# Kernel optimization log

Hardware: AMD Instinct MI355X
Metric: run time of the kernel (lower is better)

Reference implementation:

```python
import jax, jax.numpy as jnp
import numpy as np

N_SUB = 4  # fixed RK4 substeps per timestep (stands in for adaptive dopri5)
HID, IN, OUT = 64, 16, 1


def setup_inputs() -> dict:
    key = jax.random.key(0)
    ks = jax.random.split(key, 8)
    B, S = 512, 1024
    return {
        "x": jax.random.normal(ks[0], (B, S, IN), dtype=jnp.float32),
        "W_in": jax.random.normal(ks[1], (HID, IN), dtype=jnp.float32) * 0.1,
        "b_in": jnp.zeros((HID,), dtype=jnp.float32),
        "W_hh": jax.random.normal(ks[2], (HID, HID), dtype=jnp.float32) * 0.01,
        "W_ih": jax.random.normal(ks[3], (HID, HID), dtype=jnp.float32) * 0.01,
        "bias": jnp.zeros((HID,), dtype=jnp.float32),
        "tau": jnp.ones((HID,), dtype=jnp.float32),
        "W_out": jax.random.normal(ks[4], (OUT, HID), dtype=jnp.float32) * 0.1,
        "b_out": jnp.zeros((OUT,), dtype=jnp.float32),
    }


def _forward(x, W_in, b_in, W_hh, W_ih, bias, tau, W_out, b_out):
    B, S, _ = x.shape
    t_pts = jnp.linspace(0.0, 1.0, S).astype(x.dtype)
    # dt for step 0 is t[0] (=0), then successive differences, as in the torch code
    dts = jnp.concatenate([t_pts[:1], t_pts[1:] - t_pts[:-1]])

    def ode_f(h, inp):
        # dh/dt = (-h + tanh(h) W_hh^T + inp W_ih^T + bias) / tau
        return (-h + jnp.tanh(h) @ W_hh.T + inp + bias) / tau

    def step(h, xs):
        x_t, dt = xs
        inp = (x_t @ W_in.T + b_in) @ W_ih.T  # input_layer then W_ih effect
        hsub = dt / N_SUB

        def rk4(i, h):
            k1 = ode_f(h, inp)
            k2 = ode_f(h + 0.5 * hsub * k1, inp)
            k3 = ode_f(h + 0.5 * hsub * k2, inp)
            k4 = ode_f(h + hsub * k3, inp)
            return h + (hsub / 6.0) * (k1 + 2.0 * k2 + 2.0 * k3 + k4)

        h = jax.lax.fori_loop(0, N_SUB, rk4, h)
        out = jnp.tanh(h) @ W_out.T + b_out
        return h, out

    h0 = jnp.zeros((B, HID), dtype=x.dtype)
    _, outs = jax.lax.scan(step, h0, (jnp.swapaxes(x, 0, 1), dts))  # outs: [S,B,OUT]
    return jnp.swapaxes(outs, 0, 1)  # [B,S,OUT]


def reference(x, W_in, b_in, W_hh, W_ih, bias, tau, W_out, b_out):
    return _forward(x, W_in, b_in, W_hh, W_ih, bias, tau, W_out, b_out)
```

## Files before the change

### kernel.cpp

```cpp
#include <hip/hip_runtime.h>


constexpr int HID  = 64;
constexpr int INF  = 16;
constexpr int SLEN = 1024;
constexpr int BATCH = 512;
constexpr int K    = 128;
constexpr int NPIC = 2;
constexpr int TFS  = HID + 8;
constexpr int GS   = HID + 4;

typedef __fp16 h2_t   __attribute__((ext_vector_type(2)));
typedef __fp16 f16x8_t __attribute__((ext_vector_type(8)));
typedef float  f32x4_t __attribute__((ext_vector_type(4)));

#if __has_builtin(__builtin_amdgcn_mfma_f32_16x16x32_f16)
#define HAVE_MFMA16 1
#else
#define HAVE_MFMA16 0
#endif

__device__ __forceinline__ float fdot(unsigned a, h2_t w, float acc) {
    return __builtin_amdgcn_fdot2(__builtin_bit_cast(h2_t, a), w, acc, false);
}

__device__ __forceinline__ float fast_tanh(float x) {
    float e = __builtin_amdgcn_exp2f(x * 2.8853900817779268f);
    float r = __builtin_amdgcn_rcpf(e + 1.0f);
    return fmaf(-2.0f, r, 1.0f);
}

__device__ __forceinline__ float beta_of(float z) {
    return z * (1.0f - z * (0.5f - z * ((1.0f/6.0f) - z * (1.0f/24.0f))));
}

__global__ __launch_bounds__(512) void lnn_picard2_kernel(
    const float* __restrict__ x,
    const float* __restrict__ W_in,
    const float* __restrict__ b_in,
    const float* __restrict__ W_hh,
    const float* __restrict__ W_ih,
    const float* __restrict__ bias,
    const float* __restrict__ tau,
    const float* __restrict__ W_out,
    const float* __restrict__ b_out,
    float* __restrict__ out)
{
    const int tid  = threadIdx.x;
    const int lane = tid & 63;
    const int wid  = tid >> 6;
    const int b    = blockIdx.x;
    const int kg   = lane >> 4;
    const int ln   = lane & 15;

    __shared__ __fp16 Tf[K][TFS];
    __shared__ float  G [K][GS];

    float Wc[INF];
    #pragma unroll
    for (int k = 0; k < INF; ++k) Wc[k] = 0.0f;
    float bcomb = 0.0f;
    for (int j = 0; j < HID; ++j) {
        float wij = W_ih[lane * HID + j];
        bcomb = fmaf(wij, b_in[j], bcomb);
        #pragma unroll
        for (int k = 0; k < INF; ++k) Wc[k] = fmaf(wij, W_in[j * INF + k], Wc[k]);
    }
    const float cbase = bcomb + bias[lane];
    const float bo    = b_out[0];
    const float wo    = W_out[lane];

    const float hsub  = 1.0f / 1023.0f;
    const float rtau  = 1.0f / tau[lane];
    const float beta  = beta_of(hsub * rtau);
    const float alpha = 1.0f - beta;
    float aa2 = alpha * alpha, aa4 = aa2 * aa2, aa8 = aa4 * aa4;
    const float a16 = aa8 * aa8;

    bool mfok = false;
#if HAVE_MFMA16
    f16x8_t Bw[4][2];
    {
        #pragma unroll
        for (int m = 0; m < 16; ++m) {
            int j = 16 * wid + m;
            Tf[j][lane] = (__fp16)(float)(((j * 5 + lane * 3) & 7) - 3);
        }
        #pragma unroll
        for (int c = 0; c < 4; ++c)
            #pragma unroll
            for (int kc = 0; kc < 2; ++kc) {
                int col = 16 * c + ln;
                #pragma unroll
                for (int e = 0; e < 8; ++e) {
                    int m = 32 * kc + 8 * kg + e;
                    Bw[c][kc][e] = (__fp16)(float)(((col * 3 + m * 7) & 7) - 3);
                }
            }
        __syncthreads();
        {
            f32x4_t acc[4];
            #pragma unroll
            for (int c = 0; c < 4; ++c) acc[c] = (f32x4_t){0.f, 0.f, 0.f, 0.f};
            const uint4* rowp = (const uint4*)(&Tf[16 * wid + ln][0]);
            #pragma unroll
            for (int kc = 0; kc < 2; ++kc) {
                f16x8_t A = __builtin_bit_cast(f16x8_t, rowp[4 * kc + kg]);
                #pragma unroll
                for (int c = 0; c < 4; ++c)
                    acc[c] = __builtin_amdgcn_mfma_f32_16x16x32_f16(
                        A, Bw[c][kc], acc[c], 0, 0, 0);
            }
            #pragma unroll
            for (int c = 0; c < 4; ++c)
                #pragma unroll
                for (int r = 0; r < 4; ++r)
                    G[16 * wid + 4 * kg + r][16 * c + ln] = acc[c][r];
        }
        int ok = 1;
        for (int m = 0; m < 16; ++m) {
            int j = 16 * wid + m;
            int ref = 0;
            for (int mm = 0; mm < HID; ++mm)
                ref += (((lane * 3 + mm * 7) & 7) - 3)
                     * (((j * 5 + mm * 3) & 7) - 3);
            ok &= (G[j][lane] == (float)ref);
        }
        mfok = (__syncthreads_and(ok) != 0);
        if (mfok) {
            #pragma unroll
            for (int c = 0; c < 4; ++c) {
                int col = 16 * c + ln;
                float bcol = beta_of(hsub * (1.0f / tau[col]));
                #pragma unroll
                for (int kc = 0; kc < 2; ++kc)
                    #pragma unroll
                    for (int e = 0; e < 8; ++e) {
                        int m = 32 * kc + 8 * kg + e;
                        Bw[c][kc][e] = (__fp16)(W_hh[col * HID + m] * bcol);
                    }
            }
        }
    }
#endif
    h2_t wh[HID / 2];
    if (!mfok) {
        const float4* w4 = (const float4*)(W_hh + lane * HID);
        #pragma unroll
        for (int q = 0; q < HID / 4; ++q) {
            float4 v = w4[q];
            wh[2*q+0] = __builtin_amdgcn_cvt_pkrtz(v.x * beta, v.y * beta);
            wh[2*q+1] = __builtin_amdgcn_cvt_pkrtz(v.z * beta, v.w * beta);
        }
    }

    if (tid == 0) out[(size_t)b * SLEN] = bo;

    float h0 = 0.0f;
    float cbreg[16];

    for (int ch = 0; ch < (SLEN - 1 + K - 1) / K; ++ch) {
        const int sbase = ch * K + 1;
        const int ns    = min(K, (SLEN - 1) - ch * K);

        {
            __fp16 t0 = (__fp16)fast_tanh(h0);
            #pragma unroll
            for (int m = 0; m < 16; ++m) {
                int j = 16 * wid + m;
                if (j < ns) {
                    const float4* xs =
                        (const float4*)(x + ((size_t)b * SLEN + sbase + j) * INF);
                    float4 p0 = xs[0], p1 = xs[1], p2 = xs[2], p3 = xs[3];
                    float cA = fmaf(p0.x, Wc[0], fmaf(p0.y, Wc[1],
                               fmaf(p0.z, Wc[2], fmaf(p0.w, Wc[3], cbase))));
                    float cB = fmaf(p1.x, Wc[4], fmaf(p1.y, Wc[5],
                               fmaf(p1.z, Wc[6], p1.w * Wc[7])));
                    float cC = fmaf(p2.x, Wc[8], fmaf(p2.y, Wc[9],
                               fmaf(p2.z, Wc[10], p2.w * Wc[11])));
                    float cD = fmaf(p3.x, Wc[12], fmaf(p3.y, Wc[13],
                               fmaf(p3.z, Wc[14], p3.w * Wc[15])));
                    cbreg[m] = ((cA + cB) + (cC + cD)) * beta;
                    Tf[j][lane] = t0;
                }
            }
        }
        __syncthreads();

        for (int it = 0; it < NPIC; ++it) {
#if HAVE_MFMA16
            if (mfok) {
                f32x4_t acc[4];
                #pragma unroll
                for (int c = 0; c < 4; ++c) acc[c] = (f32x4_t){0.f,0.f,0.f,0.f};
                const uint4* rowp = (const uint4*)(&Tf[16 * wid + ln][0]);
                #pragma unroll
                for (int kc = 0; kc < 2; ++kc) {
                    f16x8_t A = __builtin_bit_cast(f16x8_t, rowp[4 * kc + kg]);
                    #pragma unroll
                    for (int c = 0; c < 4; ++c)
                        acc[c] = __builtin_amdgcn_mfma_f32_16x16x32_f16(
                            A, Bw[c][kc], acc[c], 0, 0, 0);
                }
                #pragma unroll
                for (int c = 0; c < 4; ++c)
                    #pragma unroll
                    for (int r = 0; r < 4; ++r)
                        G[16 * wid + 4 * kg + r][16 * c + ln] = acc[c][r];
            } else
#endif
            {
                for (int m = 0; m < 16; ++m) {
                    int j = 16 * wid + m;
                    if (j < ns) {
                        const uint4* t4 = (const uint4*)Tf[j];
                        float a0 = 0.f, a1 = 0.f, a2_ = 0.f, a3 = 0.f;
                        #pragma unroll
                        for (int q = 0; q < 8; ++q) {
                            uint4 r = t4[q];
                            a0  = fdot(r.x, wh[4*q+0], a0);
                            a1  = fdot(r.y, wh[4*q+1], a1);
                            a2_ = fdot(r.z, wh[4*q+2], a2_);
                            a3  = fdot(r.w, wh[4*q+3], a3);
                        }
                        G[j][lane] = (a0 + a1) + (a2_ + a3);
                    }
                }
            }
            {
                float L = 0.0f;
                #pragma unroll
                for (int m = 0; m < 16; ++m) {
                    int j = 16 * wid + m;
                    if (j < ns) {
                        L = fmaf(alpha, L, G[j][lane] + cbreg[m]);
                        G[j][lane] = L;
                    }
                }
            }
            __syncthreads();
            {
                float E = h0;
                for (int w = 0; w < wid; ++w)
                    E = fmaf(a16, E, G[16 * w + 15][lane]);
                float p = alpha;
                #pragma unroll
                for (int m = 0; m < 16; ++m) {
                    int j = 16 * wid + m;
                    if (j < ns) {
                        float H = fmaf(p, E, G[j][lane]);
                        G[j][lane] = H;
                        if (it < NPIC - 1 && j + 1 < ns)
                            Tf[j + 1][lane] = (__fp16)fast_tanh(H);
                    }
                    p *= alpha;
                }
            }
            __syncthreads();
        }

        for (int m = 0; m < 16; ++m) {
            int j = 16 * wid + m;
            if (j < ns) {
                float t = (float)(__fp16)fast_tanh(G[j][lane]);
                float v = t * wo;
                #pragma unroll
                for (int mm = 32; mm >= 1; mm >>= 1) v += __shfl_xor(v, mm, 64);
                if (lane == 0) out[(size_t)b * SLEN + sbase + j] = v + bo;
            }
        }
        h0 = G[ns - 1][lane];
        __syncthreads();
    }
}

extern "C" void kernel_launch(void* const* d_in, const int* in_sizes, int n_in,
                              void* d_out, int out_size, void* d_ws, size_t ws_size,
                              hipStream_t stream) {
    const float* x     = (const float*)d_in[0];
    const float* W_in  = (const float*)d_in[1];
    const float* b_in  = (const float*)d_in[2];
    const float* W_hh  = (const float*)d_in[3];
    const float* W_ih  = (const float*)d_in[4];
    const float* bias  = (const float*)d_in[5];
    const float* tau   = (const float*)d_in[6];
    const float* W_out = (const float*)d_in[7];
    const float* b_out = (const float*)d_in[8];
    float* out = (float*)d_out;

    lnn_picard2_kernel<<<BATCH, 512, 0, stream>>>(
        x, W_in, b_in, W_hh, W_ih, bias, tau, W_out, b_out, out);
}
```

Before: 333.2 us.

## Halve block size and replace first Picard sweep with constant-gradient scan

Blocks drop from 512 to 256 threads, so each wave now owns 32 timesteps instead of 16. The first Picard iteration no longer runs a full MFMA pass over all rows. Instead, each wave computes one fdot2 matvec from tanh(h0) at its first row and reuses that gradient for the whole segment. The output projection is fused into the final scan pass, and the carry is passed through a small shared buffer. Together these remove one MFMA sweep plus a barrier per chunk, at the cost of a longer serial scan per wave, lower per-block parallelism, and different numerics in the first iterate.

```diff
diff --git a/kernel.cpp b/kernel.cpp
--- a/kernel.cpp
+++ b/kernel.cpp
@@ -6,7 +6,7 @@
 constexpr int SLEN = 1024;
 constexpr int BATCH = 512;
 constexpr int K    = 128;
-constexpr int NPIC = 2;
+constexpr int NS_W = 32;
 constexpr int TFS  = HID + 8;
 constexpr int GS   = HID + 4;
 
@@ -34,7 +34,7 @@
     return z * (1.0f - z * (0.5f - z * ((1.0f/6.0f) - z * (1.0f/24.0f))));
 }
 
-__global__ __launch_bounds__(512) void lnn_picard2_kernel(
+__global__ __launch_bounds__(256) void lnn_picard3_kernel(
     const float* __restrict__ x,
     const float* __restrict__ W_in,
     const float* __restrict__ b_in,
@@ -52,9 +52,11 @@
     const int b    = blockIdx.x;
     const int kg   = lane >> 4;
     const int ln   = lane & 15;
+    const int jb   = NS_W * wid;
 
     __shared__ __fp16 Tf[K][TFS];
     __shared__ float  G [K][GS];
+    __shared__ float  hcar[HID];
 
     float Wc[INF];
     #pragma unroll
@@ -75,15 +77,27 @@
     const float beta  = beta_of(hsub * rtau);
     const float alpha = 1.0f - beta;
     float aa2 = alpha * alpha, aa4 = aa2 * aa2, aa8 = aa4 * aa4;
-    const float a16 = aa8 * aa8;
+    float aa16 = aa8 * aa8;
+    const float a32 = aa16 * aa16;
+
+    h2_t wh[HID / 2];
+    {
+        const float4* w4 = (const float4*)(W_hh + lane * HID);
+        #pragma unroll
+        for (int q = 0; q < HID / 4; ++q) {
+            float4 v = w4[q];
+            wh[2*q+0] = __builtin_amdgcn_cvt_pkrtz(v.x * beta, v.y * beta);
+            wh[2*q+1] = __builtin_amdgcn_cvt_pkrtz(v.z * beta, v.w * beta);
+        }
+    }
 
     bool mfok = false;
 #if HAVE_MFMA16
     f16x8_t Bw[4][2];
     {
         #pragma unroll
-        for (int m = 0; m < 16; ++m) {
-            int j = 16 * wid + m;
+        for (int m = 0; m < NS_W; ++m) {
+            int j = jb + m;
             Tf[j][lane] = (__fp16)(float)(((j * 5 + lane * 3) & 7) - 3);
         }
         #pragma unroll
@@ -98,11 +112,12 @@
                 }
             }
         __syncthreads();
-        {
+        #pragma unroll
+        for (int rg = 0; rg < 2; ++rg) {
             f32x4_t acc[4];
             #pragma unroll
             for (int c = 0; c < 4; ++c) acc[c] = (f32x4_t){0.f, 0.f, 0.f, 0.f};
-            const uint4* rowp = (const uint4*)(&Tf[16 * wid + ln][0]);
+            const uint4* rowp = (const uint4*)(&Tf[jb + 16 * rg + ln][0]);
             #pragma unroll
             for (int kc = 0; kc < 2; ++kc) {
                 f16x8_t A = __builtin_bit_cast(f16x8_t, rowp[4 * kc + kg]);
@@ -115,11 +130,11 @@
             for (int c = 0; c < 4; ++c)
                 #pragma unroll
                 for (int r = 0; r < 4; ++r)
-                    G[16 * wid + 4 * kg + r][16 * c + ln] = acc[c][r];
+                    G[jb + 16 * rg + 4 * kg + r][16 * c + ln] = acc[c][r];
         }
         int ok = 1;
-        for (int m = 0; m < 16; ++m) {
-            int j = 16 * wid + m;
+        for (int m = 0; m < NS_W; ++m) {
+            int j = jb + m;
             int ref = 0;
             for (int mm = 0; mm < HID; ++mm)
                 ref += (((lane * 3 + mm * 7) & 7) - 3)
@@ -143,31 +158,20 @@
         }
     }
 #endif
-    h2_t wh[HID / 2];
-    if (!mfok) {
-        const float4* w4 = (const float4*)(W_hh + lane * HID);
-        #pragma unroll
-        for (int q = 0; q < HID / 4; ++q) {
-            float4 v = w4[q];
-            wh[2*q+0] = __builtin_amdgcn_cvt_pkrtz(v.x * beta, v.y * beta);
-            wh[2*q+1] = __builtin_amdgcn_cvt_pkrtz(v.z * beta, v.w * beta);
-        }
-    }
 
     if (tid == 0) out[(size_t)b * SLEN] = bo;
 
     float h0 = 0.0f;
-    float cbreg[16];
+    float cbreg[NS_W];
 
     for (int ch = 0; ch < (SLEN - 1 + K - 1) / K; ++ch) {
         const int sbase = ch * K + 1;
         const int ns    = min(K, (SLEN - 1) - ch * K);
 
         {
-            __fp16 t0 = (__fp16)fast_tanh(h0);
-            #pragma unroll
-            for (int m = 0; m < 16; ++m) {
-                int j = 16 * wid + m;
+            #pragma unroll
+            for (int m = 0; m < NS_W; ++m) {
+                int j = jb + m;
                 if (j < ns) {
                     const float4* xs =
                         (const float4*)(x + ((size_t)b * SLEN + sbase + j) * INF);
@@ -181,19 +185,61 @@
                     float cD = fmaf(p3.x, Wc[12], fmaf(p3.y, Wc[13],
                                fmaf(p3.z, Wc[14], p3.w * Wc[15])));
                     cbreg[m] = ((cA + cB) + (cC + cD)) * beta;
-                    Tf[j][lane] = t0;
-                }
-            }
-        }
-        __syncthreads();
-
-        for (int it = 0; it < NPIC; ++it) {
+                }
+            }
+            Tf[jb][lane] = (__fp16)fast_tanh(h0);
+        }
+
+        {
+            const uint4* t4 = (const uint4*)Tf[jb];
+            float a0 = 0.f, a1 = 0.f, a2_ = 0.f, a3 = 0.f;
+            #pragma unroll
+            for (int q = 0; q < 8; ++q) {
+                uint4 r = t4[q];
+                a0  = fdot(r.x, wh[4*q+0], a0);
+                a1  = fdot(r.y, wh[4*q+1], a1);
+                a2_ = fdot(r.z, wh[4*q+2], a2_);
+                a3  = fdot(r.w, wh[4*q+3], a3);
+            }
+            float g0 = (a0 + a1) + (a2_ + a3);
+            float L = 0.0f;
+            #pragma unroll
+            for (int m = 0; m < NS_W; ++m) {
+                int j = jb + m;
+                if (j < ns) {
+                    L = fmaf(alpha, L, g0 + cbreg[m]);
+                    G[j][lane] = L;
+                }
+            }
+        }
+        __syncthreads();
+
+        {
+            float E = h0;
+            for (int w = 0; w < wid; ++w)
+                E = fmaf(a32, E, G[NS_W * w + NS_W - 1][lane]);
+            float p = alpha;
+            #pragma unroll
+            for (int m = 0; m < NS_W; ++m) {
+                int j = jb + m;
+                if (j < ns) {
+                    float H = fmaf(p, E, G[j][lane]);
+                    if (j + 1 < ns)
+                        Tf[j + 1][lane] = (__fp16)fast_tanh(H);
+                }
+                p *= alpha;
+            }
+        }
+        __syncthreads();
+
 #if HAVE_MFMA16
-            if (mfok) {
+        if (mfok) {
+            #pragma unroll
+            for (int rg = 0; rg < 2; ++rg) {
                 f32x4_t acc[4];
                 #pragma unroll
                 for (int c = 0; c < 4; ++c) acc[c] = (f32x4_t){0.f,0.f,0.f,0.f};
-                const uint4* rowp = (const uint4*)(&Tf[16 * wid + ln][0]);
+                const uint4* rowp = (const uint4*)(&Tf[jb + 16 * rg + ln][0]);
                 #pragma unroll
                 for (int kc = 0; kc < 2; ++kc) {
                     f16x8_t A = __builtin_bit_cast(f16x8_t, rowp[4 * kc + kg]);
@@ -206,71 +252,64 @@
                 for (int c = 0; c < 4; ++c)
                     #pragma unroll
                     for (int r = 0; r < 4; ++r)
-                        G[16 * wid + 4 * kg + r][16 * c + ln] = acc[c][r];
-            } else
+                        G[jb + 16 * rg + 4 * kg + r][16 * c + ln] = acc[c][r];
+            }
+        } else
 #endif
-            {
-                for (int m = 0; m < 16; ++m) {
-                    int j = 16 * wid + m;
-                    if (j < ns) {
-                        const uint4* t4 = (const uint4*)Tf[j];
-                        float a0 = 0.f, a1 = 0.f, a2_ = 0.f, a3 = 0.f;
-                        #pragma unroll
-                        for (int q = 0; q < 8; ++q) {
-                            uint4 r = t4[q];
-                            a0  = fdot(r.x, wh[4*q+0], a0);
-                            a1  = fdot(r.y, wh[4*q+1], a1);
-                            a2_ = fdot(r.z, wh[4*q+2], a2_);
-                            a3  = fdot(r.w, wh[4*q+3], a3);
-                        }
-                        G[j][lane] = (a0 + a1) + (a2_ + a3);
+        {
+            for (int m = 0; m < NS_W; ++m) {
+                int j = jb + m;
+                if (j < ns) {
+                    const uint4* t4 = (const uint4*)Tf[j];
+                    float a0 = 0.f, a1 = 0.f, a2_ = 0.f, a3 = 0.f;
+                    #pragma unroll
+                    for (int q = 0; q < 8; ++q) {
+                        uint4 r = t4[q];
+                        a0  = fdot(r.x, wh[4*q+0], a0);
+                        a1  = fdot(r.y, wh[4*q+1], a1);
+                        a2_ = fdot(r.z, wh[4*q+2], a2_);
+                        a3  = fdot(r.w, wh[4*q+3], a3);
                     }
-                }
-            }
-            {
-                float L = 0.0f;
-                #pragma unroll
-                for (int m = 0; m < 16; ++m) {
-                    int j = 16 * wid + m;
-                    if (j < ns) {
-                        L = fmaf(alpha, L, G[j][lane] + cbreg[m]);
-                        G[j][lane] = L;
-                    }
-                }
-            }
-            __syncthreads();
-            {
-                float E = h0;
-                for (int w = 0; w < wid; ++w)
-                    E = fmaf(a16, E, G[16 * w + 15][lane]);
-                float p = alpha;
-                #pragma unroll
-                for (int m = 0; m < 16; ++m) {
-                    int j = 16 * wid + m;
-                    if (j < ns) {
-                        float H = fmaf(p, E, G[j][lane]);
-                        G[j][lane] = H;
-                        if (it < NPIC - 1 && j + 1 < ns)
-                            Tf[j + 1][lane] = (__fp16)fast_tanh(H);
-                    }
-                    p *= alpha;
-                }
-            }
-            __syncthreads();
-        }
-
-        for (int m = 0; m < 16; ++m) {
-            int j = 16 * wid + m;
-            if (j < ns) {
-                float t = (float)(__fp16)fast_tanh(G[j][lane]);
-                float v = t * wo;
-                #pragma unroll
-                for (int mm = 32; mm >= 1; mm >>= 1) v += __shfl_xor(v, mm, 64);
-                if (lane == 0) out[(size_t)b * SLEN + sbase + j] = v + bo;
-            }
-        }
-        h0 = G[ns - 1][lane];
-        __syncthreads();
+                    G[j][lane] = (a0 + a1) + (a2_ + a3);
+                }
+            }
+        }
+        {
+            float L = 0.0f;
+            #pragma unroll
+            for (int m = 0; m < NS_W; ++m) {
+                int j = jb + m;
+                if (j < ns) {
+                    L = fmaf(alpha, L, G[j][lane] + cbreg[m]);
+                    G[j][lane] = L;
+                }
+            }
+        }
+        __syncthreads();
+
+        {
+            float E = h0;
+            for (int w = 0; w < wid; ++w)
+                E = fmaf(a32, E, G[NS_W * w + NS_W - 1][lane]);
+            float p = alpha;
+            #pragma unroll
+            for (int m = 0; m < NS_W; ++m) {
+                int j = jb + m;
+                if (j < ns) {
+                    float H = fmaf(p, E, G[j][lane]);
+                    float t = (float)(__fp16)fast_tanh(H);
+                    float v = t * wo;
+                    #pragma unroll
+                    for (int mm = 32; mm >= 1; mm >>= 1)
+                        v += __shfl_xor(v, mm, 64);
+                    if (lane == 0) out[(size_t)b * SLEN + sbase + j] = v + bo;
+                    if (j == ns - 1) hcar[lane] = H;
+                }
+                p *= alpha;
+            }
+        }
+        __syncthreads();
+        h0 = hcar[lane];
     }
 }
 
@@ -288,6 +327,6 @@
     const float* b_out = (const float*)d_in[8];
     float* out = (float*)d_out;
 
-    lnn_picard2_kernel<<<BATCH, 512, 0, stream>>>(
+    lnn_picard3_kernel<<<BATCH, 256, 0, stream>>>(
         x, W_in, b_in, W_hh, W_ih, bias, tau, W_out, b_out, out);
 }
```

After: 470.0 us. 41.1% more time.
